# Kernel tuning notes

Hardware: AMD Instinct MI355X
Metric: run time of the kernel (lower is better)

Reference implementation:

```python
import jax, jax.numpy as jnp
import numpy as np


def setup_inputs() -> dict:
    key = jax.random.key(0)
    ks = jax.random.split(key, 10)
    B, C, D, H, W = 2, 512, 8, 32, 32
    Ck = C // 4  # shared KV head dim (and fixed query dim per intended MQA math)
    s = 0.02
    return {
        "x": jax.random.normal(ks[0], (B, C, D, H, W), dtype=jnp.float32),
        "Wq": jax.random.normal(ks[1], (Ck, C), dtype=jnp.float32) * s,
        "bq": jnp.zeros((Ck,), dtype=jnp.float32),
        "Wk": jax.random.normal(ks[2], (Ck, C), dtype=jnp.float32) * s,
        "bk": jnp.zeros((Ck,), dtype=jnp.float32),
        "Wv": jax.random.normal(ks[3], (Ck, C), dtype=jnp.float32) * s,
        "bv": jnp.zeros((Ck,), dtype=jnp.float32),
        "Wo": jax.random.normal(ks[4], (C, C), dtype=jnp.float32) * s,
        "bo": jnp.zeros((C,), dtype=jnp.float32),
    }


def reference(x, Wq, bq, Wk, bk, Wv, bv, Wo, bo):
    B, C, D, H, W = x.shape
    N = D * H * W
    Ck = Wk.shape[0]  # C // 4
    xf = x.reshape(B, C, N)  # flatten spatial dims -> sequence axis
    # 1x1 Conv3d == per-voxel linear projection over channels
    q = jnp.einsum('oc,bcn->bno', Wq, xf) + bq  # [B, N, Ck]
    k = jnp.einsum('oc,bcn->bno', Wk, xf) + bk  # [B, N, Ck]
    v = jnp.einsum('oc,bcn->bno', Wv, xf) + bv  # [B, N, Ck]
    scale = jnp.asarray(Ck, x.dtype) ** -0.5
    attn = jax.nn.softmax(jnp.einsum('bnc,bmc->bnm', q, k) * scale, axis=-1)  # [B, N, N]
    out = jnp.einsum('bnm,bmc->bnc', attn, v)  # [B, N, Ck]
    out = jnp.tile(out, (1, 1, 4))  # repeat(1,1,4) -> [B, N, C]
    out = jnp.einsum('oc,bnc->bon', Wo, out) + bo[None, :, None]  # [B, C, N]
    return out.reshape(B, C, D, H, W) + x
```

## Files before the change

### kernel.cpp

```cpp
#include <hip/hip_runtime.h>
#include <hip/hip_bf16.h>

typedef __bf16 bf16;
typedef __bf16 bf16x8 __attribute__((ext_vector_type(8)));
typedef __bf16 bf16x4 __attribute__((ext_vector_type(4)));
typedef float  f32x4  __attribute__((ext_vector_type(4)));

constexpr int BB = 2, C = 512, NN = 8192, CK = 128;

__global__ __launch_bounds__(256) void k_qkv(
    const float* __restrict__ x,
    const float* __restrict__ Wq, const float* __restrict__ bq,
    const float* __restrict__ Wk, const float* __restrict__ bk,
    const float* __restrict__ Wv, const float* __restrict__ bv,
    bf16* __restrict__ qkv_ws)
{
    const int t = threadIdx.x;
    const int lane = t & 63, w = t >> 6;
    const int lr = lane & 15, lg = lane >> 4;
    const int n0 = blockIdx.x * 128;
    const int which = blockIdx.y;
    const int b = blockIdx.z;
    const float* W    = which == 0 ? Wq : (which == 1 ? Wk : Wv);
    const float* bias = which == 0 ? bq : (which == 1 ? bk : bv);
    bf16* out = qkv_ws + (size_t)which * BB * NN * CK;

    __shared__ __align__(16) char s_xT[128 * 144];
    __shared__ __align__(16) char s_w [128 * 144];

    f32x4 acc[2][8];
#pragma unroll
    for (int m = 0; m < 2; m++)
#pragma unroll
        for (int j = 0; j < 8; j++) acc[m][j] = (f32x4){0.f, 0.f, 0.f, 0.f};

    const float* xb = x + (size_t)b * C * NN;

    const int tok4 = (t & 31) * 4;
    const int c8   = (t >> 5) * 8;
    const int ob   = t >> 2;
    const int c16  = (t & 3) * 16;

    for (int kt = 0; kt < C; kt += 64) {
        __syncthreads();
        {
            float4 v[8];
#pragma unroll
            for (int i = 0; i < 8; i++)
                v[i] = *(const float4*)(xb + (size_t)(kt + c8 + i) * NN + n0 + tok4);
#pragma unroll
            for (int j = 0; j < 4; j++) {
                int tok = tok4 + j;
                bf16x8 pk = { (bf16)v[0].x, (bf16)v[1].x, (bf16)v[2].x, (bf16)v[3].x,
                              (bf16)v[4].x, (bf16)v[5].x, (bf16)v[6].x, (bf16)v[7].x };
                if (j == 1) pk = (bf16x8){ (bf16)v[0].y, (bf16)v[1].y, (bf16)v[2].y, (bf16)v[3].y,
                                           (bf16)v[4].y, (bf16)v[5].y, (bf16)v[6].y, (bf16)v[7].y };
                if (j == 2) pk = (bf16x8){ (bf16)v[0].z, (bf16)v[1].z, (bf16)v[2].z, (bf16)v[3].z,
                                           (bf16)v[4].z, (bf16)v[5].z, (bf16)v[6].z, (bf16)v[7].z };
                if (j == 3) pk = (bf16x8){ (bf16)v[0].w, (bf16)v[1].w, (bf16)v[2].w, (bf16)v[3].w,
                                           (bf16)v[4].w, (bf16)v[5].w, (bf16)v[6].w, (bf16)v[7].w };
                int off = tok * 144 + ((c8 * 2) ^ ((((tok >> 2) & 7)) << 4));
                *(bf16x8*)(s_xT + off) = pk;
            }
        }
#pragma unroll
        for (int p = 0; p < 2; p++) {
            int o = ob + p * 64;
            const float* wp = W + (size_t)o * C + kt + c16;
            float4 a0 = *(const float4*)(wp);
            float4 a1 = *(const float4*)(wp + 4);
            float4 a2 = *(const float4*)(wp + 8);
            float4 a3 = *(const float4*)(wp + 12);
            bf16x8 p0 = { (bf16)a0.x, (bf16)a0.y, (bf16)a0.z, (bf16)a0.w,
                          (bf16)a1.x, (bf16)a1.y, (bf16)a1.z, (bf16)a1.w };
            bf16x8 p1 = { (bf16)a2.x, (bf16)a2.y, (bf16)a2.z, (bf16)a2.w,
                          (bf16)a3.x, (bf16)a3.y, (bf16)a3.z, (bf16)a3.w };
            int perm = ((o >> 2) & 7) << 4;
            *(bf16x8*)(s_w + o * 144 + ((c16 * 2) ^ perm)) = p0;
            *(bf16x8*)(s_w + o * 144 + ((c16 * 2 + 16) ^ perm)) = p1;
        }
        __syncthreads();
#pragma unroll
        for (int ks = 0; ks < 2; ks++) {
            bf16x8 af[2];
#pragma unroll
            for (int m = 0; m < 2; m++) {
                int row = w * 32 + m * 16 + lr;
                af[m] = *(const bf16x8*)(s_xT + row * 144 + ((ks * 64 + lg * 16) ^ ((((row >> 2) & 7)) << 4)));
            }
#pragma unroll
            for (int j = 0; j < 8; j++) {
                int row = j * 16 + lr;
                bf16x8 bfr = *(const bf16x8*)(s_w + row * 144 + ((ks * 64 + lg * 16) ^ ((((row >> 2) & 7)) << 4)));
                acc[0][j] = __builtin_amdgcn_mfma_f32_16x16x32_bf16(af[0], bfr, acc[0][j], 0, 0, 0);
                acc[1][j] = __builtin_amdgcn_mfma_f32_16x16x32_bf16(af[1], bfr, acc[1][j], 0, 0, 0);
            }
        }
    }
#pragma unroll
    for (int m = 0; m < 2; m++)
#pragma unroll
        for (int j = 0; j < 8; j++) {
            int o = j * 16 + lr;
            float bia = bias[o];
#pragma unroll
            for (int r = 0; r < 4; r++) {
                int tok = n0 + w * 32 + m * 16 + lg * 4 + r;
                out[((size_t)b * NN + tok) * CK + o] = (bf16)(acc[m][j][r] + bia);
            }
        }
}

__global__ __launch_bounds__(512, 4) void k_attn(
    const bf16* __restrict__ qkv_ws,
    float* __restrict__ Opart, float* __restrict__ Mw, float* __restrict__ Lw,
    int nsplit)
{
    const int t = threadIdx.x;
    const int lane = t & 63, w = t >> 6;
    const int lr = lane & 15, lg = lane >> 4;

    const int total = 64 * BB * nsplit;
    const int chunkv = total >> 3;
    const int lin = blockIdx.x;
    const int rid = (lin & 7) * chunkv + (lin >> 3);
    const int qt = rid & 63;
    const int bs = rid >> 6;
    const int b = bs & 1, split = bs >> 1;

    const int q0 = qt * 128;
    const int kbeg = split * (NN / nsplit);
    const int nt = (NN / nsplit) / 64;

    const bf16* qg = qkv_ws;
    const bf16* kg = qkv_ws + (size_t)BB * NN * CK;
    const bf16* vg = qkv_ws + (size_t)2 * BB * NN * CK;

    __shared__ __align__(16) char s_k[2][64 * 256];
    __shared__ __align__(16) char s_vt[2][128 * 128];
    __shared__ __align__(16) char s_p[8][16 * 80];

    const float scale = 0.08838834764831845f;
    const float L2E = 1.4426950408889634f;

    const int kread_base = (lr * 256 + lg * 16) ^ ((lr & 7) << 4);
    int vb[8];
#pragma unroll
    for (int dj = 0; dj < 8; dj++) {
        int d = dj * 16 + lr;
        vb[dj] = (d * 128 + lg * 16) ^ (((d ^ (d >> 3)) & 7) << 4);
    }
    char* s_pw = s_p[w];

    const int t2 = t & 255;
    const int sc = t2 & 15;
    const int sr = t2 >> 4;
    const int kw_base = (sr * 256 + sc * 16) ^ ((sr & 7) << 4);
    const int vw_base = (sc * 1024 + sr * 8) ^ ((sc & 7) << 4);

    bf16x8 qf[4];
    {
        float qs = scale * L2E;
        const bf16* qp = qg + ((size_t)b * NN + q0 + w * 16 + lr) * CK;
#pragma unroll
        for (int ks = 0; ks < 4; ks++) {
            bf16x8 v = *(const bf16x8*)(qp + ks * 32 + lg * 8);
#pragma unroll
            for (int i = 0; i < 8; i++) qf[ks][i] = (bf16)((float)v[i] * qs);
        }
    }

    f32x4 oacc[8];
#pragma unroll
    for (int dj = 0; dj < 8; dj++) oacc[dj] = (f32x4){0.f, 0.f, 0.f, 0.f};
    float mrun = 0.f, lrun = 0.f;

    const bf16* kp = kg + ((size_t)b * NN + kbeg + sr) * CK + sc * 8;
    const bf16* vp = vg + ((size_t)b * NN + kbeg + sr * 4) * CK + sc * 8;
    bf16x8 stg[4];

    auto issue_loads = [&]() {
        if (w < 4) {
#pragma unroll
            for (int p = 0; p < 4; p++) stg[p] = *(const bf16x8*)(kp + (size_t)(16 * p) * CK);
        } else {
#pragma unroll
            for (int p = 0; p < 4; p++) stg[p] = *(const bf16x8*)(vp + (size_t)p * CK);
        }
        kp += (size_t)64 * CK;
        vp += (size_t)64 * CK;
    };

    issue_loads();

    for (int it = 0; it < nt; it++) {
        const int buf = it & 1;
        if (w < 4) {
            char* skw = s_k[buf] + kw_base;
#pragma unroll
            for (int p = 0; p < 4; p++)
                *(bf16x8*)(skw + p * 4096) = stg[p];
        } else {
            char* svw = s_vt[buf];
#pragma unroll
            for (int i = 0; i < 8; i++) {
                bf16x4 pk = { stg[0][i], stg[1][i], stg[2][i], stg[3][i] };
                *(bf16x4*)(svw + (vw_base ^ (i * 144))) = pk;
            }
        }
        __syncthreads();
        if (it + 1 < nt) issue_loads();

        const char* sv = s_vt[buf];

        f32x4 sa[4];
        __builtin_amdgcn_s_setprio(1);
#pragma unroll
        for (int j = 0; j < 4; j++) {
            sa[j] = (f32x4){0.f, 0.f, 0.f, 0.f};
#pragma unroll
            for (int ks = 0; ks < 4; ks++) {
                bf16x8 kf = *(const bf16x8*)(s_k[buf] + ((kread_base ^ (ks * 64)) + j * 4096));
                sa[j] = __builtin_amdgcn_mfma_f32_16x16x32_bf16(kf, qf[ks], sa[j], 0, 0, 0);
            }
        }
        __builtin_amdgcn_s_setprio(0);

        float m0 = fmaxf(fmaxf(sa[0][0], sa[0][1]), fmaxf(sa[0][2], sa[0][3]));
        float m1 = fmaxf(fmaxf(sa[1][0], sa[1][1]), fmaxf(sa[1][2], sa[1][3]));
        float m2 = fmaxf(fmaxf(sa[2][0], sa[2][1]), fmaxf(sa[2][2], sa[2][3]));
        float m3 = fmaxf(fmaxf(sa[3][0], sa[3][1]), fmaxf(sa[3][2], sa[3][3]));
        float pmax = fmaxf(fmaxf(m0, m1), fmaxf(m2, m3));
        bool ok = (pmax <= mrun + 8.f);
        if (!__all(ok)) {
            float mx = pmax;
            mx = fmaxf(mx, __shfl_xor(mx, 16));
            mx = fmaxf(mx, __shfl_xor(mx, 32));
            float mnew = fmaxf(mrun, mx);
            float corr = exp2f(mrun - mnew);
            mrun = mnew;
            lrun *= corr;
            float co[4];
#pragma unroll
            for (int r = 0; r < 4; r++)
                co[r] = __shfl(corr, (lane & 48) | (lg * 4 + r));
#pragma unroll
            for (int dj = 0; dj < 8; dj++)
#pragma unroll
                for (int r = 0; r < 4; r++) oacc[dj][r] *= co[r];
        }

        {
            float ps = 0.f;
#pragma unroll
            for (int j = 0; j < 4; j++) {
                float p0 = exp2f(sa[j][0] - mrun);
                float p1 = exp2f(sa[j][1] - mrun);
                float p2 = exp2f(sa[j][2] - mrun);
                float p3 = exp2f(sa[j][3] - mrun);
                ps += (p0 + p1) + (p2 + p3);
                bf16x4 pk = { (bf16)p0, (bf16)p1, (bf16)p2, (bf16)p3 };
                *(bf16x4*)(s_pw + lr * 80 + lg * 8 + j * 32) = pk;
            }
            lrun += ps;
        }

        __builtin_amdgcn_s_setprio(1);
#pragma unroll
        for (int kc = 0; kc < 2; kc++) {
            bf16x8 pf = *(const bf16x8*)(s_pw + lr * 80 + lg * 16 + kc * 64);
#pragma unroll
            for (int dj = 0; dj < 8; dj++) {
                bf16x8 vf = *(const bf16x8*)(sv + (vb[dj] ^ (kc * 64)));
                oacc[dj] = __builtin_amdgcn_mfma_f32_16x16x32_bf16(pf, vf, oacc[dj], 0, 0, 0);
            }
        }
        __builtin_amdgcn_s_setprio(0);
    }

    size_t obase = ((size_t)split * BB + b) * NN;
    int qbase = q0 + w * 16;
    {
        float ls = lrun;
        ls += __shfl_xor(ls, 16);
        ls += __shfl_xor(ls, 32);
        if (lg == 0) {
            Mw[obase + qbase + lr] = mrun;
            Lw[obase + qbase + lr] = ls;
        }
#pragma unroll
        for (int dj = 0; dj < 8; dj++)
#pragma unroll
            for (int r = 0; r < 4; r++) {
                int q = qbase + lg * 4 + r;
                Opart[(obase + q) * CK + dj * 16 + lr] = oacc[dj][r];
            }
    }
}

__global__ __launch_bounds__(256) void k_combine(
    const float* __restrict__ Opart, const float* __restrict__ Mw,
    const float* __restrict__ Lw, bf16* __restrict__ ao, int nsplit)
{
    const int t = threadIdx.x;
    const int b = blockIdx.y;
    const int r0 = blockIdx.x * 64;
    const int d4 = (t & 31) * 4;
#pragma unroll
    for (int p = 0; p < 8; p++) {
        int row = r0 + (t >> 5) + p * 8;
        size_t rbase = (size_t)b * NN + row;
        float M = -1e30f;
        for (int s = 0; s < nsplit; s++)
            M = fmaxf(M, Mw[((size_t)s * BB) * NN + rbase]);
        float L = 0.f;
        float4 acc = {0.f, 0.f, 0.f, 0.f};
        for (int s = 0; s < nsplit; s++) {
            size_t sb = ((size_t)s * BB) * NN + rbase;
            float wgt = exp2f(Mw[sb] - M);
            L += Lw[sb] * wgt;
            float4 v = *(const float4*)(Opart + sb * CK + d4);
            acc.x += v.x * wgt; acc.y += v.y * wgt;
            acc.z += v.z * wgt; acc.w += v.w * wgt;
        }
        float inv = 1.f / L;
        bf16x4 o4 = { (bf16)(acc.x * inv), (bf16)(acc.y * inv),
                      (bf16)(acc.z * inv), (bf16)(acc.w * inv) };
        *(bf16x4*)(ao + rbase * CK + d4) = o4;
    }
}

__global__ __launch_bounds__(256) void k_out(
    const float* __restrict__ x, const float* __restrict__ Wo, const float* __restrict__ bo,
    const bf16* __restrict__ ao, float* __restrict__ y)
{
    const int t = threadIdx.x;
    const int lane = t & 63, w = t >> 6;
    const int lr = lane & 15, lg = lane >> 4;
    const int n0 = blockIdx.x * 128;
    const int o0 = blockIdx.y * 64;
    const int b = blockIdx.z;

    __shared__ __align__(16) char s_w[64 * 256];
    __shared__ __align__(16) char s_a[128 * 256];

    {
        int c4 = (t & 31) * 4, rbase = t >> 5;
#pragma unroll
        for (int p = 0; p < 8; p++) {
            int row = rbase + p * 8;
            const float* wp = Wo + (size_t)(o0 + row) * C + c4;
            float4 a0 = *(const float4*)(wp);
            float4 a1 = *(const float4*)(wp + 128);
            float4 a2 = *(const float4*)(wp + 256);
            float4 a3 = *(const float4*)(wp + 384);
            bf16x4 r4 = { (bf16)(a0.x + a1.x + a2.x + a3.x), (bf16)(a0.y + a1.y + a2.y + a3.y),
                          (bf16)(a0.z + a1.z + a2.z + a3.z), (bf16)(a0.w + a1.w + a2.w + a3.w) };
            int off = (row * 256 + c4 * 2) ^ ((row & 7) << 4);
            *(bf16x4*)(s_w + off) = r4;
        }
    }
    {
        int chunk = t & 15, rbase = t >> 4;
#pragma unroll
        for (int p = 0; p < 8; p++) {
            int row = rbase + p * 16;
            bf16x8 v = *(const bf16x8*)(ao + ((size_t)b * NN + n0 + row) * CK + chunk * 8);
            int off = (row * 256 + chunk * 16) ^ ((row & 7) << 4);
            *(bf16x8*)(s_a + off) = v;
        }
    }
    __syncthreads();

    f32x4 acc[8];
#pragma unroll
    for (int j = 0; j < 8; j++) acc[j] = (f32x4){0.f, 0.f, 0.f, 0.f};
#pragma unroll
    for (int ks = 0; ks < 4; ks++) {
        int row = w * 16 + lr;
        int aoff = (row * 256 + (ks * 32 + lg * 8) * 2) ^ ((row & 7) << 4);
        bf16x8 wf = *(const bf16x8*)(s_w + aoff);
#pragma unroll
        for (int j = 0; j < 8; j++) {
            int nrow = j * 16 + lr;
            int boff = (nrow * 256 + (ks * 32 + lg * 8) * 2) ^ ((nrow & 7) << 4);
            bf16x8 af = *(const bf16x8*)(s_a + boff);
            acc[j] = __builtin_amdgcn_mfma_f32_16x16x32_bf16(wf, af, acc[j], 0, 0, 0);
        }
    }
#pragma unroll
    for (int j = 0; j < 8; j++) {
        int n = n0 + j * 16 + lr;
#pragma unroll
        for (int r = 0; r < 4; r++) {
            int o = o0 + w * 16 + lg * 4 + r;
            size_t idx = ((size_t)b * C + o) * NN + n;
            y[idx] = acc[j][r] + bo[o] + x[idx];
        }
    }
}

extern "C" void kernel_launch(void* const* d_in, const int* in_sizes, int n_in,
                              void* d_out, int out_size, void* d_ws, size_t ws_size,
                              hipStream_t stream)
{
    const float* x  = (const float*)d_in[0];
    const float* Wq = (const float*)d_in[1];
    const float* bq = (const float*)d_in[2];
    const float* Wk = (const float*)d_in[3];
    const float* bk = (const float*)d_in[4];
    const float* Wv = (const float*)d_in[5];
    const float* bv = (const float*)d_in[6];
    const float* Wo = (const float*)d_in[7];
    const float* bo = (const float*)d_in[8];
    float* y = (float*)d_out;

    const size_t qkv_elems = (size_t)3 * BB * NN * CK;
    const size_t ao_elems  = (size_t)BB * NN * CK;

    bf16* qkv = (bf16*)d_ws;
    bf16* ao  = qkv + qkv_elems;
    float* Opart = (float*)(ao + ao_elems);

    int nsplit = 4;
    {
        size_t fixed = (qkv_elems + ao_elems) * sizeof(bf16);
        size_t per_split = ((size_t)BB * NN * CK + 2 * (size_t)BB * NN) * sizeof(float);
        while (nsplit > 1 && fixed + (size_t)nsplit * per_split > ws_size) nsplit >>= 1;
    }
    float* Mw = Opart + (size_t)nsplit * BB * NN * CK;
    float* Lw = Mw + (size_t)nsplit * BB * NN;

    k_qkv<<<dim3(NN / 128, 3, BB), 256, 0, stream>>>(x, Wq, bq, Wk, bk, Wv, bv, qkv);
    k_attn<<<dim3(64 * BB * nsplit, 1, 1), 512, 0, stream>>>(qkv, Opart, Mw, Lw, nsplit);
    k_combine<<<dim3(NN / 64, BB), 256, 0, stream>>>(Opart, Mw, Lw, ao, nsplit);
    k_out<<<dim3(NN / 128, C / 64, BB), 256, 0, stream>>>(x, Wo, bo, ao, y);
}
```

Measured before the change: 167.0 us.

## Switch attention to 32x32x16 MFMA with register-resident P via permlane swap

The attention kernel moves from 16x16x32 to 32x32x16 bf16 MFMA tiles, so each wave handles 32 query rows and a block covers 256 queries. The probability matrix P is no longer sent through shared memory. It is packed with v_cvt_pk_bf16_f32 and rearranged in registers with v_permlane32_swap so it can feed the PV MFMA directly. The aim is to raise K/V reuse per shared-memory load, remove the LDS round trip for P, and cut the rowmax shuffles. In exchange the accumulators need more registers, occupancy drops to 2 blocks per SM, and there are half as many blocks in the grid.

```diff
diff --git a/kernel.cpp b/kernel.cpp
--- a/kernel.cpp
+++ b/kernel.cpp
@@ -5,8 +5,20 @@
 typedef __bf16 bf16x8 __attribute__((ext_vector_type(8)));
 typedef __bf16 bf16x4 __attribute__((ext_vector_type(4)));
 typedef float  f32x4  __attribute__((ext_vector_type(4)));
+typedef float  f32x16 __attribute__((ext_vector_type(16)));
+typedef unsigned int u32;
+typedef u32 u32x4 __attribute__((ext_vector_type(4)));
 
 constexpr int BB = 2, C = 512, NN = 8192, CK = 128;
+
+__device__ __forceinline__ u32 cvt_pk_bf16(float lo, float hi) {
+    u32 r;
+    asm("v_cvt_pk_bf16_f32 %0, %1, %2" : "=v"(r) : "v"(lo), "v"(hi));
+    return r;
+}
+__device__ __forceinline__ void pl32_swap(u32& a, u32& b) {
+    asm("v_permlane32_swap_b32 %0, %1" : "+v"(a), "+v"(b));
+}
 
 __global__ __launch_bounds__(256) void k_qkv(
     const float* __restrict__ x,
@@ -111,68 +123,62 @@
         }
 }
 
-__global__ __launch_bounds__(512, 4) void k_attn(
+__global__ __launch_bounds__(512, 2) void k_attn(
     const bf16* __restrict__ qkv_ws,
     float* __restrict__ Opart, float* __restrict__ Mw, float* __restrict__ Lw,
     int nsplit)
 {
     const int t = threadIdx.x;
     const int lane = t & 63, w = t >> 6;
-    const int lr = lane & 15, lg = lane >> 4;
-
-    const int total = 64 * BB * nsplit;
+    const int lq = lane & 31, hi = lane >> 5;
+
+    const int total = 32 * BB * nsplit;
     const int chunkv = total >> 3;
     const int lin = blockIdx.x;
     const int rid = (lin & 7) * chunkv + (lin >> 3);
-    const int qt = rid & 63;
-    const int bs = rid >> 6;
+    const int qt = rid & 31;
+    const int bs = rid >> 5;
     const int b = bs & 1, split = bs >> 1;
 
-    const int q0 = qt * 128;
+    const int q0 = qt * 256;
     const int kbeg = split * (NN / nsplit);
     const int nt = (NN / nsplit) / 64;
 
-    const bf16* qg = qkv_ws;
     const bf16* kg = qkv_ws + (size_t)BB * NN * CK;
     const bf16* vg = qkv_ws + (size_t)2 * BB * NN * CK;
 
     __shared__ __align__(16) char s_k[2][64 * 256];
     __shared__ __align__(16) char s_vt[2][128 * 128];
-    __shared__ __align__(16) char s_p[8][16 * 80];
-
-    const float scale = 0.08838834764831845f;
-    const float L2E = 1.4426950408889634f;
-
-    const int kread_base = (lr * 256 + lg * 16) ^ ((lr & 7) << 4);
-    int vb[8];
-#pragma unroll
-    for (int dj = 0; dj < 8; dj++) {
-        int d = dj * 16 + lr;
-        vb[dj] = (d * 128 + lg * 16) ^ (((d ^ (d >> 3)) & 7) << 4);
-    }
-    char* s_pw = s_p[w];
-
+
+    const int kb0 = lq * 256 + ((((lq & 7) ^ hi)) << 4);
+    int vbs[4];
+#pragma unroll
+    for (int db = 0; db < 4; db++) {
+        int d = db * 32 + lq;
+        vbs[db] = d * 128 + (((((d ^ (d >> 3)) & 7) ^ hi)) << 4);
+    }
     const int t2 = t & 255;
-    const int sc = t2 & 15;
-    const int sr = t2 >> 4;
+    const int sc = t2 & 15, sr = t2 >> 4;
     const int kw_base = (sr * 256 + sc * 16) ^ ((sr & 7) << 4);
     const int vw_base = (sc * 1024 + sr * 8) ^ ((sc & 7) << 4);
 
-    bf16x8 qf[4];
+    bf16x8 qf[8];
     {
-        float qs = scale * L2E;
-        const bf16* qp = qg + ((size_t)b * NN + q0 + w * 16 + lr) * CK;
-#pragma unroll
-        for (int ks = 0; ks < 4; ks++) {
-            bf16x8 v = *(const bf16x8*)(qp + ks * 32 + lg * 8);
+        const float qs = 0.08838834764831845f * 1.4426950408889634f;
+        const bf16* qp = qkv_ws + ((size_t)b * NN + q0 + w * 32 + lq) * CK + hi * 8;
+#pragma unroll
+        for (int ks = 0; ks < 8; ks++) {
+            bf16x8 v = *(const bf16x8*)(qp + ks * 16);
 #pragma unroll
             for (int i = 0; i < 8; i++) qf[ks][i] = (bf16)((float)v[i] * qs);
         }
     }
 
-    f32x4 oacc[8];
-#pragma unroll
-    for (int dj = 0; dj < 8; dj++) oacc[dj] = (f32x4){0.f, 0.f, 0.f, 0.f};
+    f32x16 oacc[4];
+#pragma unroll
+    for (int db = 0; db < 4; db++)
+#pragma unroll
+        for (int i = 0; i < 16; i++) oacc[db][i] = 0.f;
     float mrun = 0.f, lrun = 0.f;
 
     const bf16* kp = kg + ((size_t)b * NN + kbeg + sr) * CK + sc * 8;
@@ -211,90 +217,97 @@
         __syncthreads();
         if (it + 1 < nt) issue_loads();
 
+        const char* sk = s_k[buf];
         const char* sv = s_vt[buf];
 
-        f32x4 sa[4];
+        f32x16 sa0, sa1;
+#pragma unroll
+        for (int i = 0; i < 16; i++) { sa0[i] = 0.f; sa1[i] = 0.f; }
         __builtin_amdgcn_s_setprio(1);
 #pragma unroll
-        for (int j = 0; j < 4; j++) {
-            sa[j] = (f32x4){0.f, 0.f, 0.f, 0.f};
-#pragma unroll
-            for (int ks = 0; ks < 4; ks++) {
-                bf16x8 kf = *(const bf16x8*)(s_k[buf] + ((kread_base ^ (ks * 64)) + j * 4096));
-                sa[j] = __builtin_amdgcn_mfma_f32_16x16x32_bf16(kf, qf[ks], sa[j], 0, 0, 0);
-            }
+        for (int ks = 0; ks < 8; ks++) {
+            bf16x8 kf0 = *(const bf16x8*)(sk + (kb0 ^ (ks * 32)));
+            bf16x8 kf1 = *(const bf16x8*)(sk + ((kb0 ^ (ks * 32)) + 8192));
+            sa0 = __builtin_amdgcn_mfma_f32_32x32x16_bf16(kf0, qf[ks], sa0, 0, 0, 0);
+            sa1 = __builtin_amdgcn_mfma_f32_32x32x16_bf16(kf1, qf[ks], sa1, 0, 0, 0);
         }
         __builtin_amdgcn_s_setprio(0);
 
-        float m0 = fmaxf(fmaxf(sa[0][0], sa[0][1]), fmaxf(sa[0][2], sa[0][3]));
-        float m1 = fmaxf(fmaxf(sa[1][0], sa[1][1]), fmaxf(sa[1][2], sa[1][3]));
-        float m2 = fmaxf(fmaxf(sa[2][0], sa[2][1]), fmaxf(sa[2][2], sa[2][3]));
-        float m3 = fmaxf(fmaxf(sa[3][0], sa[3][1]), fmaxf(sa[3][2], sa[3][3]));
-        float pmax = fmaxf(fmaxf(m0, m1), fmaxf(m2, m3));
+        float m8[8];
+#pragma unroll
+        for (int i = 0; i < 8; i++) m8[i] = fmaxf(sa0[i], sa0[i + 8]);
+#pragma unroll
+        for (int i = 0; i < 8; i++) m8[i] = fmaxf(m8[i], fmaxf(sa1[i], sa1[i + 8]));
+        float pmax = fmaxf(fmaxf(fmaxf(m8[0], m8[1]), fmaxf(m8[2], m8[3])),
+                           fmaxf(fmaxf(m8[4], m8[5]), fmaxf(m8[6], m8[7])));
+        pmax = fmaxf(pmax, __shfl_xor(pmax, 32));
         bool ok = (pmax <= mrun + 8.f);
         if (!__all(ok)) {
-            float mx = pmax;
-            mx = fmaxf(mx, __shfl_xor(mx, 16));
-            mx = fmaxf(mx, __shfl_xor(mx, 32));
-            float mnew = fmaxf(mrun, mx);
+            float mnew = fmaxf(mrun, pmax);
             float corr = exp2f(mrun - mnew);
             mrun = mnew;
             lrun *= corr;
-            float co[4];
-#pragma unroll
-            for (int r = 0; r < 4; r++)
-                co[r] = __shfl(corr, (lane & 48) | (lg * 4 + r));
-#pragma unroll
-            for (int dj = 0; dj < 8; dj++)
-#pragma unroll
-                for (int r = 0; r < 4; r++) oacc[dj][r] *= co[r];
-        }
-
+#pragma unroll
+            for (int r = 0; r < 16; r++) {
+                int qrow = (r & 3) + 8 * (r >> 2) + 4 * hi;
+                float co = __shfl(corr, qrow);
+#pragma unroll
+                for (int db = 0; db < 4; db++) oacc[db][r] *= co;
+            }
+        }
+
+        f32x16 p0, p1;
+#pragma unroll
+        for (int i = 0; i < 16; i++) { p0[i] = exp2f(sa0[i] - mrun); p1[i] = exp2f(sa1[i] - mrun); }
         {
-            float ps = 0.f;
-#pragma unroll
-            for (int j = 0; j < 4; j++) {
-                float p0 = exp2f(sa[j][0] - mrun);
-                float p1 = exp2f(sa[j][1] - mrun);
-                float p2 = exp2f(sa[j][2] - mrun);
-                float p3 = exp2f(sa[j][3] - mrun);
-                ps += (p0 + p1) + (p2 + p3);
-                bf16x4 pk = { (bf16)p0, (bf16)p1, (bf16)p2, (bf16)p3 };
-                *(bf16x4*)(s_pw + lr * 80 + lg * 8 + j * 32) = pk;
-            }
-            lrun += ps;
-        }
+            float s0 = ((p0[0] + p0[1]) + (p0[2] + p0[3])) + ((p0[4] + p0[5]) + (p0[6] + p0[7]));
+            float s1 = ((p0[8] + p0[9]) + (p0[10] + p0[11])) + ((p0[12] + p0[13]) + (p0[14] + p0[15]));
+            float s2 = ((p1[0] + p1[1]) + (p1[2] + p1[3])) + ((p1[4] + p1[5]) + (p1[6] + p1[7]));
+            float s3 = ((p1[8] + p1[9]) + (p1[10] + p1[11])) + ((p1[12] + p1[13]) + (p1[14] + p1[15]));
+            lrun += (s0 + s1) + (s2 + s3);
+        }
+        u32 W0[8], W1[8];
+#pragma unroll
+        for (int j = 0; j < 8; j++) {
+            W0[j] = cvt_pk_bf16(p0[2 * j], p0[2 * j + 1]);
+            W1[j] = cvt_pk_bf16(p1[2 * j], p1[2 * j + 1]);
+        }
+        pl32_swap(W0[0], W0[2]); pl32_swap(W0[1], W0[3]);
+        pl32_swap(W0[4], W0[6]); pl32_swap(W0[5], W0[7]);
+        pl32_swap(W1[0], W1[2]); pl32_swap(W1[1], W1[3]);
+        pl32_swap(W1[4], W1[6]); pl32_swap(W1[5], W1[7]);
 
         __builtin_amdgcn_s_setprio(1);
 #pragma unroll
-        for (int kc = 0; kc < 2; kc++) {
-            bf16x8 pf = *(const bf16x8*)(s_pw + lr * 80 + lg * 16 + kc * 64);
-#pragma unroll
-            for (int dj = 0; dj < 8; dj++) {
-                bf16x8 vf = *(const bf16x8*)(sv + (vb[dj] ^ (kc * 64)));
-                oacc[dj] = __builtin_amdgcn_mfma_f32_16x16x32_bf16(pf, vf, oacc[dj], 0, 0, 0);
+        for (int s = 0; s < 4; s++) {
+            u32x4 fw;
+            if (s == 0)      fw = (u32x4){W0[0], W0[1], W0[2], W0[3]};
+            else if (s == 1) fw = (u32x4){W0[4], W0[5], W0[6], W0[7]};
+            else if (s == 2) fw = (u32x4){W1[0], W1[1], W1[2], W1[3]};
+            else             fw = (u32x4){W1[4], W1[5], W1[6], W1[7]};
+            bf16x8 pa = __builtin_bit_cast(bf16x8, fw);
+            const int coff = (s >> 1) * 64 + (s & 1) * 32;
+#pragma unroll
+            for (int db = 0; db < 4; db++) {
+                bf16x8 vf = *(const bf16x8*)(sv + (vbs[db] ^ coff));
+                oacc[db] = __builtin_amdgcn_mfma_f32_32x32x16_bf16(pa, vf, oacc[db], 0, 0, 0);
             }
         }
         __builtin_amdgcn_s_setprio(0);
     }
 
-    size_t obase = ((size_t)split * BB + b) * NN;
-    int qbase = q0 + w * 16;
-    {
-        float ls = lrun;
-        ls += __shfl_xor(ls, 16);
-        ls += __shfl_xor(ls, 32);
-        if (lg == 0) {
-            Mw[obase + qbase + lr] = mrun;
-            Lw[obase + qbase + lr] = ls;
-        }
-#pragma unroll
-        for (int dj = 0; dj < 8; dj++)
-#pragma unroll
-            for (int r = 0; r < 4; r++) {
-                int q = qbase + lg * 4 + r;
-                Opart[(obase + q) * CK + dj * 16 + lr] = oacc[dj][r];
-            }
+    size_t obase = (((size_t)split * BB + b) * NN + q0 + w * 32);
+    float ls = lrun + __shfl_xor(lrun, 32);
+    if (lane < 32) {
+        Mw[obase + lq] = mrun;
+        Lw[obase + lq] = ls;
+    }
+#pragma unroll
+    for (int r = 0; r < 16; r++) {
+        int qrow = (r & 3) + 8 * (r >> 2) + 4 * hi;
+        float* op = Opart + (obase + qrow) * CK + lq;
+#pragma unroll
+        for (int db = 0; db < 4; db++) op[db * 32] = oacc[db][r];
     }
 }
 
@@ -432,7 +445,7 @@
     float* Lw = Mw + (size_t)nsplit * BB * NN;
 
     k_qkv<<<dim3(NN / 128, 3, BB), 256, 0, stream>>>(x, Wq, bq, Wk, bk, Wv, bv, qkv);
-    k_attn<<<dim3(64 * BB * nsplit, 1, 1), 512, 0, stream>>>(qkv, Opart, Mw, Lw, nsplit);
+    k_attn<<<dim3(32 * BB * nsplit, 1, 1), 512, 0, stream>>>(qkv, Opart, Mw, Lw, nsplit);
     k_combine<<<dim3(NN / 64, BB), 256, 0, stream>>>(Opart, Mw, Lw, ao, nsplit);
     k_out<<<dim3(NN / 128, C / 64, BB), 256, 0, stream>>>(x, Wo, bo, ao, y);
 }
```

After: 155.4 us. 1.07x faster.
